# Performance work log

Hardware: AMD Instinct MI355X
Metric: run time of the kernel (lower is better)

Reference implementation:

```python
import jax, jax.numpy as jnp
import numpy as np
from jax import lax

B, N = 8, 8192
H, W = 512, 512
C = 192          # backbone feature channels (Swin-L stage 1)
HF, WF = 128, 128  # H/4, W/4
STATE = 256
VLR = 3
STRIDE = 4.0
DOWN = 4.0
EPS = 1e-8


def bilinear_sample(feat, poly, h, w):
    """F.grid_sample(align_corners=True, bilinear) equivalent.
    feat: (B,C,h,w), poly: (B,N,2) pixel coords -> (B,C,N)."""
    gx = poly[..., 0] / (w / 2.0) - 1.0
    gy = poly[..., 1] / (h / 2.0) - 1.0
    x = (gx + 1.0) * 0.5 * (w - 1)   # align_corners=True unnormalize
    y = (gy + 1.0) * 0.5 * (h - 1)
    x0 = jnp.floor(x); y0 = jnp.floor(y)
    fx = x - x0; fy = y - y0
    x0i = jnp.clip(x0, 0, w - 1).astype(jnp.int32)
    x1i = jnp.clip(x0 + 1, 0, w - 1).astype(jnp.int32)
    y0i = jnp.clip(y0, 0, h - 1).astype(jnp.int32)
    y1i = jnp.clip(y0 + 1, 0, h - 1).astype(jnp.int32)
    b = jnp.arange(feat.shape[0])[:, None]
    f00 = feat[b, :, y0i, x0i]  # (B,N,C)
    f01 = feat[b, :, y0i, x1i]
    f10 = feat[b, :, y1i, x0i]
    f11 = feat[b, :, y1i, x1i]
    w00 = ((1 - fy) * (1 - fx))[..., None]
    w01 = ((1 - fy) * fx)[..., None]
    w10 = (fy * (1 - fx))[..., None]
    w11 = (fy * fx)[..., None]
    out = f00 * w00 + f01 * w01 + f10 * w10 + f11 * w11  # (B,N,C)
    return jnp.transpose(out, (0, 2, 1))  # (B,C,N)


def mlp3(x, W1, b1, W2, b2, W3, b3):
    """per-point MLP (1x1 conv stack). x: (B,Cin,N) -> (B,Cout,N)."""
    h1 = jax.nn.relu(jnp.einsum('oc,bcn->bon', W1, x) + b1[None, :, None])
    h2 = jax.nn.relu(jnp.einsum('oc,bcn->bon', W2, h1) + b2[None, :, None])
    return jnp.einsum('oc,bcn->bon', W3, h2) + b3[None, :, None]


def can_poly(poly, mask):
    # canonical poly: subtract per-polygon masked min of valid points
    big = jnp.float32(1e9)
    masked = jnp.where(mask[..., None] > 0, poly, big)
    mins = jnp.min(masked, axis=1, keepdims=True)  # (B,1,2)
    return (poly - mins) * mask[..., None]


def polygon_angles(poly, mask):
    prev = jnp.roll(poly, 1, axis=1)
    nxt = jnp.roll(poly, -1, axis=1)
    v1 = prev - poly
    v2 = nxt - poly
    dot = jnp.sum(v1 * v2, axis=-1)
    nrm = jnp.linalg.norm(v1, axis=-1) * jnp.linalg.norm(v2, axis=-1)
    cosang = jnp.clip(dot / (nrm + EPS), -1.0, 1.0)
    return jnp.arccos(cosang) * mask  # (B,N)


def setup_inputs() -> dict:
    key = jax.random.key(0)
    ks = jax.random.split(key, 20)
    DIN_OFF = C + 2   # 194
    DIN_CLS = C + 3   # 195
    inp = {
        'image': jax.random.normal(ks[0], (B, 3, H, W), jnp.float32),
        'pred_points': jax.random.uniform(ks[1], (B, N, 2), jnp.float32) * (WF - 1),
        'valid_mask': jnp.ones((B, N), jnp.float32),
        'bw': jax.random.normal(ks[2], (C, 3, 4, 4), jnp.float32) * 0.05,
        'bb': jnp.zeros((C,), jnp.float32),
        'off_W1': jax.random.normal(ks[3], (VLR, STATE, DIN_OFF), jnp.float32) * 0.02,
        'off_b1': jnp.zeros((VLR, STATE), jnp.float32),
        'off_W2': jax.random.normal(ks[4], (VLR, STATE, STATE), jnp.float32) * 0.02,
        'off_b2': jnp.zeros((VLR, STATE), jnp.float32),
        'off_W3': jax.random.normal(ks[5], (VLR, 2, STATE), jnp.float32) * 0.02,
        'off_b3': jnp.zeros((VLR, 2), jnp.float32),
        'cls_W1': jax.random.normal(ks[6], (STATE, DIN_CLS), jnp.float32) * 0.02,
        'cls_b1': jnp.zeros((STATE,), jnp.float32),
        'cls_W2': jax.random.normal(ks[7], (STATE, STATE), jnp.float32) * 0.02,
        'cls_b2': jnp.zeros((STATE,), jnp.float32),
        'cls_W3': jax.random.normal(ks[8], (1, STATE), jnp.float32) * 0.02,
        'cls_b3': jnp.zeros((1,), jnp.float32),
    }
    return inp


def reference(image, pred_points, valid_mask, bw, bb,
              off_W1, off_b1, off_W2, off_b2, off_W3, off_b3,
              cls_W1, cls_b1, cls_W2, cls_b2, cls_W3, cls_b3):
    # frozen backbone stand-in (torch.no_grad on swin_l): stride-4 patch-embed conv
    feat = lax.conv_general_dilated(
        image, bw, window_strides=(4, 4), padding='VALID',
        dimension_numbers=('NCHW', 'OIHW', 'NCHW')) + bb[None, :, None, None]
    feat = lax.stop_gradient(feat)  # (B,C,HF,WF)

    py = pred_points
    for i in range(VLR):
        c_py = can_poly(py, valid_mask)
        g = bilinear_sample(feat, py, HF, WF) * valid_mask[:, None, :]   # (B,C,N)
        x = jnp.concatenate([g, jnp.transpose(c_py, (0, 2, 1))], axis=1)  # (B,C+2,N)
        off = mlp3(x, off_W1[i], off_b1[i], off_W2[i], off_b2[i], off_W3[i], off_b3[i])
        off = jnp.transpose(off, (0, 2, 1)) * valid_mask[..., None]      # (B,N,2)
        py = py + off * STRIDE

    gf = bilinear_sample(feat, py, HF, WF) * valid_mask[:, None, :]      # (B,C,N)
    angles = lax.stop_gradient(polygon_angles(py, valid_mask))           # (B,N)
    cls_feat = jnp.concatenate(
        [gf, jnp.transpose(py, (0, 2, 1)), angles[:, None, :]], axis=1)  # (B,C+3,N)
    logits = mlp3(cls_feat, cls_W1, cls_b1, cls_W2, cls_b2, cls_W3, cls_b3)  # (B,1,N)
    cls_points = logits[:, 0, :] * valid_mask                            # (B,N)

    final_refined_points = py * DOWN
    return (final_refined_points, cls_points)
```

## Files before the change

### kernel.cpp

```cpp
#include <hip/hip_runtime.h>
#include <hip/hip_bf16.h>
#include <hip/hip_fp8.h>

#define NB 8
#define NP 8192
#define IMH 512
#define IMW 512
#define NC 192
#define FH 128
#define FW 128
#define NSTATE 256

#define P1 232
#define P2 264
#define K1PAD 224
#define CPITCH 72
#define W1FRAG 57344
#define W2FRAG 65536

typedef __attribute__((ext_vector_type(8))) unsigned short ush8;
typedef __attribute__((ext_vector_type(8))) short short8v;
typedef __attribute__((ext_vector_type(4))) float f32x4;

__device__ __forceinline__ float bf2f(unsigned short u) {
  return __uint_as_float(((unsigned)u) << 16);
}
__device__ __forceinline__ float fp8tof(unsigned char b) {
  __hip_fp8_e4m3 v;
  v.__x = b;
  return (float)v;
}
__device__ __forceinline__ unsigned char ftofp8(float f) {
  __hip_fp8_e4m3 v(f);
  return v.__x;
}
__device__ __forceinline__ unsigned fenc(float f) {
  unsigned u = __float_as_uint(f);
  return (u & 0x80000000u) ? ~u : (u | 0x80000000u);
}
__device__ __forceinline__ float fdec(unsigned u) {
  return __uint_as_float((u & 0x80000000u) ? (u & 0x7FFFFFFFu) : ~u);
}

__global__ __launch_bounds__(256) void conv_kernel(
    const float* __restrict__ img, const __hip_bfloat16* __restrict__ wcb,
    const float* __restrict__ bb, unsigned char* __restrict__ feat) {
  __shared__ __hip_bfloat16 Xim[64 * CPITCH];

  const int tid = threadIdx.x;
  const int lane = tid & 63;
  const int w = tid >> 6;
  const int cl = lane & 15;
  const int kg = lane >> 4;
  const int b = blockIdx.x & 7;
  const int pix0 = (blockIdx.x >> 3) * 64;
  const int y = pix0 >> 7;
  const int xh = (pix0 >> 6) & 1;

  {
    const int pix = tid & 63;
    const int q = tid >> 6;
    *(uint2*)&Xim[pix * CPITCH + 48 + q * 4] = (uint2){0u, 0u};
  }

#pragma unroll
  for (int it = 0; it < 3; ++it) {
    const int idx = it * 256 + tid;
    const int row = idx >> 6;
    const int c = idx & 63;
    const int ci = row >> 2, ky = row & 3;
    const float4 v = *(const float4*)(img + (((size_t)b * 3 + ci) * IMH +
                                             (y * 4 + ky)) * IMW + xh * 256 + c * 4);
    __hip_bfloat16 h[4];
    h[0] = __float2bfloat16(v.x);
    h[1] = __float2bfloat16(v.y);
    h[2] = __float2bfloat16(v.z);
    h[3] = __float2bfloat16(v.w);
    *(uint2*)&Xim[c * CPITCH + ci * 16 + ky * 4] = *(const uint2*)h;
  }
  __syncthreads();

  f32x4 acc[4][3];
#pragma unroll
  for (int mt = 0; mt < 4; ++mt)
#pragma unroll
    for (int nt = 0; nt < 3; ++nt) acc[mt][nt] = (f32x4){0, 0, 0, 0};

#pragma unroll
  for (int kc = 0; kc < 2; ++kc) {
    short8v af[4], bfv[3];
#pragma unroll
    for (int mt = 0; mt < 4; ++mt)
      af[mt] = *(const short8v*)&Xim[(mt * 16 + cl) * CPITCH + kc * 32 + kg * 8];
#pragma unroll
    for (int nt = 0; nt < 3; ++nt)
      bfv[nt] = *(const short8v*)&wcb[(size_t)(w * 48 + nt * 16 + cl) * 64 +
                                      kc * 32 + kg * 8];
#pragma unroll
    for (int mt = 0; mt < 4; ++mt)
#pragma unroll
      for (int nt = 0; nt < 3; ++nt)
        acc[mt][nt] = __builtin_amdgcn_mfma_f32_16x16x32_bf16(
            af[mt], bfv[nt], acc[mt][nt], 0, 0, 0);
  }

#pragma unroll
  for (int nt = 0; nt < 3; ++nt) {
    const float bias = bb[w * 48 + nt * 16 + cl];
#pragma unroll
    for (int mt = 0; mt < 4; ++mt) {
#pragma unroll
      for (int r = 0; r < 4; ++r) {
        feat[((size_t)(w * 8 + b) * 16384 + pix0 + mt * 16 + kg * 4 + r) * 48 +
             nt * 16 + cl] = ftofp8(acc[mt][nt][r] + bias);
      }
    }
  }
}

__global__ void prep_all_kernel(
    const float* __restrict__ oW1, const float* __restrict__ cW1,
    const float* __restrict__ oW2, const float* __restrict__ cW2,
    const float* __restrict__ bw, const float* __restrict__ pred,
    const float* __restrict__ mask, __hip_bfloat16* __restrict__ w1c,
    __hip_bfloat16* __restrict__ w2c, __hip_bfloat16* __restrict__ wcb,
    unsigned* __restrict__ mins4) {
  __shared__ float sx[4], sy[4];
  const int idx = blockIdx.x * 256 + threadIdx.x;
  const int region = blockIdx.y;
  if (region == 0) {
    if (idx >= 4 * W1FRAG) return;
    const int L = idx / W1FRAG;
    const int rem = idx - L * W1FRAG;
    const int kc = rem >> 13;
    const int r2 = rem & 8191;
    const int ng = r2 >> 9;
    const int r3 = r2 & 511;
    const int lane = r3 >> 3;
    const int e = r3 & 7;
    const int n = ng * 16 + (lane & 15);
    const int k = kc * 32 + (lane >> 4) * 8 + e;
    const float* src = (L < 3) ? (oW1 + (size_t)L * 256 * 194) : cW1;
    const int K = (L < 3) ? 194 : 195;
    w1c[idx] = __float2bfloat16((k < K) ? src[(size_t)n * K + k] : 0.0f);
  } else if (region == 1) {
    if (idx >= 4 * W2FRAG) return;
    const int L = idx >> 16;
    const int rem = idx & 65535;
    const int kc = rem >> 13;
    const int r2 = rem & 8191;
    const int ng = r2 >> 9;
    const int r3 = r2 & 511;
    const int lane = r3 >> 3;
    const int e = r3 & 7;
    const int n = ng * 16 + (lane & 15);
    const int k = kc * 32 + (lane >> 4) * 8 + e;
    const float* src = (L < 3) ? (oW2 + (size_t)L * 65536) : cW2;
    w2c[idx] = __float2bfloat16(src[(size_t)n * 256 + k]);
  } else if (region == 2) {
    if (idx < 48) mins4[16 + idx] = fenc(1e9f);
    if (idx >= 192 * 64) return;
    const int n = idx >> 6;
    const int k = idx & 63;
    wcb[idx] = __float2bfloat16((k < 48) ? bw[(size_t)n * 48 + k] : 0.0f);
  } else {
    if (blockIdx.x >= 8) return;
    const int b = blockIdx.x;
    float mx = 1e9f, my = 1e9f;
    for (int n = threadIdx.x; n < NP; n += 256) {
      float m = mask[(size_t)b * NP + n];
      float2 p = *(const float2*)&pred[((size_t)b * NP + n) * 2];
      mx = fminf(mx, m > 0.0f ? p.x : 1e9f);
      my = fminf(my, m > 0.0f ? p.y : 1e9f);
    }
#pragma unroll
    for (int o = 32; o > 0; o >>= 1) {
      mx = fminf(mx, __shfl_down(mx, o));
      my = fminf(my, __shfl_down(my, o));
    }
    if ((threadIdx.x & 63) == 0) {
      sx[threadIdx.x >> 6] = mx;
      sy[threadIdx.x >> 6] = my;
    }
    __syncthreads();
    if (threadIdx.x == 0) {
      mx = fminf(fminf(sx[0], sx[1]), fminf(sx[2], sx[3]));
      my = fminf(fminf(sy[0], sy[1]), fminf(sy[2], sy[3]));
      mins4[b * 2 + 0] = fenc(mx);
      mins4[b * 2 + 1] = fenc(my);
    }
  }
}

template <bool CLS>
__global__ __launch_bounds__(256, 4) void mlp_kernel(
    const unsigned char* __restrict__ feat,
    const float* __restrict__ p_in,
    const float* __restrict__ mask,
    const unsigned* __restrict__ mins_in,
    unsigned* __restrict__ mins_out,
    const __hip_bfloat16* __restrict__ W1c, const float* __restrict__ b1,
    const __hip_bfloat16* __restrict__ W2c, const float* __restrict__ b2,
    const float* __restrict__ W3, const float* __restrict__ b3,
    float* __restrict__ out0) {
  __shared__ __hip_bfloat16 Xls[64 * P2];
  __shared__ float red[4][64][2];

  const int tid = threadIdx.x;
  const int lane = tid & 63;
  const int w = tid >> 6;
  const int cl = lane & 15;
  const int kg = lane >> 4;
  const int b = blockIdx.x & 7;
  const int m0 = (blockIdx.x >> 3) * 64;

  {
    const int m = tid >> 2;
    const int j = tid & 3;
    const int n = m0 + m;
    const size_t pidx = (size_t)b * NP + n;
    const float msk = mask[pidx];
    const float2 pv = *(const float2*)&p_in[pidx * 2];
    const float px = pv.x, pyv = pv.y;
    const float xs = px * (127.0f / 128.0f);
    const float ys = pyv * (127.0f / 128.0f);
    const float x0f = floorf(xs), y0f = floorf(ys);
    const float fx = xs - x0f, fy = ys - y0f;
    const int x0 = (int)fminf(fmaxf(x0f, 0.0f), 127.0f);
    const int x1 = (int)fminf(fmaxf(x0f + 1.0f, 0.0f), 127.0f);
    const int y0 = (int)fminf(fmaxf(y0f, 0.0f), 127.0f);
    const int y1 = (int)fminf(fmaxf(y0f + 1.0f, 0.0f), 127.0f);
    const float w00 = (1.0f - fy) * (1.0f - fx);
    const float w01 = (1.0f - fy) * fx;
    const float w10 = fy * (1.0f - fx);
    const float w11 = fy * fx;
    const unsigned char* fb = feat + (size_t)(j * 8 + b) * 16384 * 48;
    const uint4* r00 = (const uint4*)(fb + (size_t)(y0 * FW + x0) * 48);
    const uint4* r01 = (const uint4*)(fb + (size_t)(y0 * FW + x1) * 48);
    const uint4* r10 = (const uint4*)(fb + (size_t)(y1 * FW + x0) * 48);
    const uint4* r11 = (const uint4*)(fb + (size_t)(y1 * FW + x1) * 48);
#pragma unroll
    for (int v = 0; v < 3; ++v) {
      union { uint4 u; unsigned char c[16]; } a0, a1, a2, a3;
      a0.u = r00[v]; a1.u = r01[v]; a2.u = r10[v]; a3.u = r11[v];
      __hip_bfloat16 h[16];
#pragma unroll
      for (int e = 0; e < 16; ++e) {
        float gg = w00 * fp8tof(a0.c[e]) + w01 * fp8tof(a1.c[e]) +
                   w10 * fp8tof(a2.c[e]) + w11 * fp8tof(a3.c[e]);
        h[e] = __float2bfloat16(gg * msk);
      }
      *(ush8*)&Xls[m * P1 + j * 48 + v * 16 + 0] = *(const ush8*)&h[0];
      *(ush8*)&Xls[m * P1 + j * 48 + v * 16 + 8] = *(const ush8*)&h[8];
    }
    if (j == 0) {
      __hip_bfloat16 ex[32];
#pragma unroll
      for (int i = 0; i < 32; ++i) ex[i] = __float2bfloat16(0.0f);
      if constexpr (!CLS) {
        ex[0] = __float2bfloat16((px - fdec(mins_in[b * 2 + 0])) * msk);
        ex[1] = __float2bfloat16((pyv - fdec(mins_in[b * 2 + 1])) * msk);
      } else {
        ex[0] = __float2bfloat16(px);
        ex[1] = __float2bfloat16(pyv);
        const int npv = (n + NP - 1) & (NP - 1);
        const int nnx = (n + 1) & (NP - 1);
        const float2 pp = *(const float2*)&p_in[((size_t)b * NP + npv) * 2];
        const float2 pn = *(const float2*)&p_in[((size_t)b * NP + nnx) * 2];
        const float v1x = pp.x - px, v1y = pp.y - pyv;
        const float v2x = pn.x - px, v2y = pn.y - pyv;
        const float dot = v1x * v2x + v1y * v2y;
        const float nrm =
            sqrtf(v1x * v1x + v1y * v1y) * sqrtf(v2x * v2x + v2y * v2y);
        const float ca = fminf(fmaxf(dot / (nrm + 1e-8f), -1.0f), 1.0f);
        ex[2] = __float2bfloat16(acosf(ca) * msk);
      }
#pragma unroll
      for (int q = 0; q < 4; ++q)
        *(ush8*)&Xls[m * P1 + 192 + q * 8] = *(const ush8*)&ex[q * 8];
    }
  }

  float b1v[4], b2v[4], w3av[4], w3bv[4];
#pragma unroll
  for (int nt = 0; nt < 4; ++nt) {
    const int n = w * 64 + nt * 16 + cl;
    b1v[nt] = b1[n];
    b2v[nt] = b2[n];
    w3av[nt] = W3[n];
    w3bv[nt] = CLS ? 0.0f : W3[256 + n];
  }
  __syncthreads();

  f32x4 acc[4][4];
#pragma unroll
  for (int mt = 0; mt < 4; ++mt)
#pragma unroll
    for (int nt = 0; nt < 4; ++nt) acc[mt][nt] = (f32x4){0, 0, 0, 0};

#pragma unroll
  for (int kc = 0; kc < 7; ++kc) {
    short8v af[4], bfv[4];
#pragma unroll
    for (int nt = 0; nt < 4; ++nt)
      bfv[nt] = *(const short8v*)&W1c[kc * 8192 + (w * 4 + nt) * 512 + lane * 8];
#pragma unroll
    for (int mt = 0; mt < 4; ++mt)
      af[mt] = *(const short8v*)&Xls[(mt * 16 + cl) * P1 + kc * 32 + kg * 8];
#pragma unroll
    for (int mt = 0; mt < 4; ++mt)
#pragma unroll
      for (int nt = 0; nt < 4; ++nt)
        acc[mt][nt] = __builtin_amdgcn_mfma_f32_16x16x32_bf16(
            af[mt], bfv[nt], acc[mt][nt], 0, 0, 0);
  }
  __syncthreads();

#pragma unroll
  for (int nt = 0; nt < 4; ++nt) {
    const float bias = b1v[nt];
    const int n = w * 64 + nt * 16 + cl;
#pragma unroll
    for (int mt = 0; mt < 4; ++mt) {
#pragma unroll
      for (int r = 0; r < 4; ++r) {
        const float v = fmaxf(acc[mt][nt][r] + bias, 0.0f);
        Xls[(mt * 16 + kg * 4 + r) * P2 + n] = __float2bfloat16(v);
      }
    }
  }
  __syncthreads();

  f32x4 acc2[4][4];
#pragma unroll
  for (int mt = 0; mt < 4; ++mt)
#pragma unroll
    for (int nt = 0; nt < 4; ++nt) acc2[mt][nt] = (f32x4){0, 0, 0, 0};

#pragma unroll
  for (int kc = 0; kc < 8; ++kc) {
    short8v af[4], bfv[4];
#pragma unroll
    for (int nt = 0; nt < 4; ++nt)
      bfv[nt] = *(const short8v*)&W2c[kc * 8192 + (w * 4 + nt) * 512 + lane * 8];
#pragma unroll
    for (int mt = 0; mt < 4; ++mt)
      af[mt] = *(const short8v*)&Xls[(mt * 16 + cl) * P2 + kc * 32 + kg * 8];
#pragma unroll
    for (int mt = 0; mt < 4; ++mt)
#pragma unroll
      for (int nt = 0; nt < 4; ++nt)
        acc2[mt][nt] = __builtin_amdgcn_mfma_f32_16x16x32_bf16(
            af[mt], bfv[nt], acc2[mt][nt], 0, 0, 0);
  }

  float pr[4][4][2];
#pragma unroll
  for (int mt = 0; mt < 4; ++mt)
#pragma unroll
    for (int r = 0; r < 4; ++r) { pr[mt][r][0] = 0.0f; pr[mt][r][1] = 0.0f; }

#pragma unroll
  for (int nt = 0; nt < 4; ++nt) {
    const float bias = b2v[nt];
    const float w3a = w3av[nt];
    const float w3b = w3bv[nt];
#pragma unroll
    for (int mt = 0; mt < 4; ++mt) {
#pragma unroll
      for (int r = 0; r < 4; ++r) {
        const float t = fmaxf(acc2[mt][nt][r] + bias, 0.0f);
        pr[mt][r][0] = fmaf(t, w3a, pr[mt][r][0]);
        if constexpr (!CLS) pr[mt][r][1] = fmaf(t, w3b, pr[mt][r][1]);
      }
    }
  }
#pragma unroll
  for (int s = 1; s < 16; s <<= 1) {
#pragma unroll
    for (int mt = 0; mt < 4; ++mt)
#pragma unroll
      for (int r = 0; r < 4; ++r) {
        pr[mt][r][0] += __shfl_xor(pr[mt][r][0], s);
        if constexpr (!CLS) pr[mt][r][1] += __shfl_xor(pr[mt][r][1], s);
      }
  }
  if constexpr (!CLS) {
    if (cl < 8) {
      const int r = cl >> 1, o = cl & 1;
#pragma unroll
      for (int mt = 0; mt < 4; ++mt)
        red[w][mt * 16 + kg * 4 + r][o] = pr[mt][r][o];
    }
  } else {
    if (cl < 4) {
      const int r = cl;
#pragma unroll
      for (int mt = 0; mt < 4; ++mt)
        red[w][mt * 16 + kg * 4 + r][0] = pr[mt][r][0];
    }
  }
  __syncthreads();

  if constexpr (!CLS) {
    if (tid < 128) {
      const int m = tid >> 1, o = tid & 1;
      const float s = red[0][m][o] + red[1][m][o] + red[2][m][o] + red[3][m][o];
      const size_t pidx = (size_t)b * NP + m0 + m;
      const float msk = mask[pidx];
      const float off = (s + b3[o]) * msk;
      const float nv = p_in[pidx * 2 + o] + off * 4.0f;
      out0[pidx * 2 + o] = nv;
      float mval = (msk > 0.0f) ? nv : 1e9f;
#pragma unroll
      for (int st = 2; st < 64; st <<= 1)
        mval = fminf(mval, __shfl_xor(mval, st));
      if ((tid & 63) < 2 && mins_out != nullptr)
        atomicMin(&mins_out[b * 2 + o], fenc(mval));
    }
  } else {
    if (tid < 64) {
      const int m = tid;
      const float s = red[0][m][0] + red[1][m][0] + red[2][m][0] + red[3][m][0];
      const size_t pidx = (size_t)b * NP + m0 + m;
      const float msk = mask[pidx];
      out0[pidx * 2 + 0] = p_in[pidx * 2 + 0] * 4.0f;
      out0[pidx * 2 + 1] = p_in[pidx * 2 + 1] * 4.0f;
      out0[(size_t)2 * NB * NP + pidx] = (s + b3[0]) * msk;
    }
  }
}

extern "C" void kernel_launch(void* const* d_in, const int* in_sizes, int n_in,
                              void* d_out, int out_size, void* d_ws,
                              size_t ws_size, hipStream_t stream) {
  const float* image = (const float*)d_in[0];
  const float* pred  = (const float*)d_in[1];
  const float* mask  = (const float*)d_in[2];
  const float* bw    = (const float*)d_in[3];
  const float* bb    = (const float*)d_in[4];
  const float* oW1   = (const float*)d_in[5];
  const float* ob1   = (const float*)d_in[6];
  const float* oW2   = (const float*)d_in[7];
  const float* ob2   = (const float*)d_in[8];
  const float* oW3   = (const float*)d_in[9];
  const float* ob3   = (const float*)d_in[10];
  const float* cW1   = (const float*)d_in[11];
  const float* cb1   = (const float*)d_in[12];
  const float* cW2   = (const float*)d_in[13];
  const float* cb2   = (const float*)d_in[14];
  const float* cW3   = (const float*)d_in[15];
  const float* cb3   = (const float*)d_in[16];
  float* out = (float*)d_out;

  char* ws = (char*)d_ws;
  unsigned char* feat = (unsigned char*)ws;
  const size_t featB = (size_t)NB * FH * FW * NC;
  float* pyA  = (float*)(ws + featB);
  float* pyB  = pyA + (size_t)NB * NP * 2;
  unsigned* mins4 = (unsigned*)(pyB + (size_t)NB * NP * 2);
  __hip_bfloat16* w1c = (__hip_bfloat16*)(mins4 + 64);
  __hip_bfloat16* w2c = w1c + (size_t)4 * W1FRAG;
  __hip_bfloat16* wcb = w2c + (size_t)4 * W2FRAG;

  prep_all_kernel<<<dim3(1024, 4), 256, 0, stream>>>(
      oW1, cW1, oW2, cW2, bw, pred, mask, w1c, w2c, wcb, mins4);
  conv_kernel<<<dim3(NB * 16384 / 64), 256, 0, stream>>>(image, wcb, bb, feat);

  const float* cur = pred;
  float* nxt = pyA;
  for (int i = 0; i < 3; ++i) {
    mlp_kernel<false><<<dim3(NB * NP / 64), 256, 0, stream>>>(
        feat, cur, mask, mins4 + i * 16,
        (i < 2) ? (mins4 + (i + 1) * 16) : nullptr,
        w1c + (size_t)i * W1FRAG, ob1 + (size_t)i * NSTATE,
        w2c + (size_t)i * W2FRAG, ob2 + (size_t)i * NSTATE,
        oW3 + (size_t)i * 2 * NSTATE, ob3 + (size_t)i * 2, nxt);
    cur = nxt;
    nxt = (nxt == pyA) ? pyB : pyA;
  }
  mlp_kernel<true><<<dim3(NB * NP / 64), 256, 0, stream>>>(
      feat, cur, mask, nullptr, nullptr, w1c + (size_t)3 * W1FRAG, cb1,
      w2c + (size_t)3 * W2FRAG, cb2, cW3, cb3, out);
}
```

Measured before the change: 221.5 us.

## Store fp8 features pixel-contiguous across all channels and lower MLP occupancy hint

The conv kernel now writes the fp8 feature map as one 192-byte record per pixel instead of four separate 48-channel planes. The gather in the MLP kernel has its four threads per point read interleaved 16-byte chunks of that record, so each corner fetch touches one contiguous row rather than four distant planes. The launch-bounds minimum-blocks hint drops from 4 to 2, which lets the compiler use more registers per thread at the cost of fewer resident waves. Dead helpers and an unused define are removed.

Result: faster. 186.7 us, median of 3 (-15.7%).

```diff
diff --git a/kernel.cpp b/kernel.cpp
--- a/kernel.cpp
+++ b/kernel.cpp
@@ -13,7 +13,6 @@
 
 #define P1 232
 #define P2 264
-#define K1PAD 224
 #define CPITCH 72
 #define W1FRAG 57344
 #define W2FRAG 65536
@@ -22,9 +21,6 @@
 typedef __attribute__((ext_vector_type(8))) short short8v;
 typedef __attribute__((ext_vector_type(4))) float f32x4;
 
-__device__ __forceinline__ float bf2f(unsigned short u) {
-  return __uint_as_float(((unsigned)u) << 16);
-}
 __device__ __forceinline__ float fp8tof(unsigned char b) {
   __hip_fp8_e4m3 v;
   v.__x = b;
@@ -111,8 +107,8 @@
     for (int mt = 0; mt < 4; ++mt) {
 #pragma unroll
       for (int r = 0; r < 4; ++r) {
-        feat[((size_t)(w * 8 + b) * 16384 + pix0 + mt * 16 + kg * 4 + r) * 48 +
-             nt * 16 + cl] = ftofp8(acc[mt][nt][r] + bias);
+        feat[((size_t)b * 16384 + pix0 + mt * 16 + kg * 4 + r) * 192 +
+             w * 48 + nt * 16 + cl] = ftofp8(acc[mt][nt][r] + bias);
       }
     }
   }
@@ -193,7 +189,7 @@
 }
 
 template <bool CLS>
-__global__ __launch_bounds__(256, 4) void mlp_kernel(
+__global__ __launch_bounds__(256, 2) void mlp_kernel(
     const unsigned char* __restrict__ feat,
     const float* __restrict__ p_in,
     const float* __restrict__ mask,
@@ -216,7 +212,7 @@
 
   {
     const int m = tid >> 2;
-    const int j = tid & 3;
+    const int s = tid & 3;
     const int n = m0 + m;
     const size_t pidx = (size_t)b * NP + n;
     const float msk = mask[pidx];
@@ -234,15 +230,18 @@
     const float w01 = (1.0f - fy) * fx;
     const float w10 = fy * (1.0f - fx);
     const float w11 = fy * fx;
-    const unsigned char* fb = feat + (size_t)(j * 8 + b) * 16384 * 48;
-    const uint4* r00 = (const uint4*)(fb + (size_t)(y0 * FW + x0) * 48);
-    const uint4* r01 = (const uint4*)(fb + (size_t)(y0 * FW + x1) * 48);
-    const uint4* r10 = (const uint4*)(fb + (size_t)(y1 * FW + x0) * 48);
-    const uint4* r11 = (const uint4*)(fb + (size_t)(y1 * FW + x1) * 48);
+    const unsigned char* fb = feat + (size_t)b * 16384 * 192 + s * 16;
+    const unsigned char* r00 = fb + (size_t)(y0 * FW + x0) * 192;
+    const unsigned char* r01 = fb + (size_t)(y0 * FW + x1) * 192;
+    const unsigned char* r10 = fb + (size_t)(y1 * FW + x0) * 192;
+    const unsigned char* r11 = fb + (size_t)(y1 * FW + x1) * 192;
 #pragma unroll
     for (int v = 0; v < 3; ++v) {
       union { uint4 u; unsigned char c[16]; } a0, a1, a2, a3;
-      a0.u = r00[v]; a1.u = r01[v]; a2.u = r10[v]; a3.u = r11[v];
+      a0.u = *(const uint4*)(r00 + v * 64);
+      a1.u = *(const uint4*)(r01 + v * 64);
+      a2.u = *(const uint4*)(r10 + v * 64);
+      a3.u = *(const uint4*)(r11 + v * 64);
       __hip_bfloat16 h[16];
 #pragma unroll
       for (int e = 0; e < 16; ++e) {
@@ -250,10 +249,10 @@
                    w10 * fp8tof(a2.c[e]) + w11 * fp8tof(a3.c[e]);
         h[e] = __float2bfloat16(gg * msk);
       }
-      *(ush8*)&Xls[m * P1 + j * 48 + v * 16 + 0] = *(const ush8*)&h[0];
-      *(ush8*)&Xls[m * P1 + j * 48 + v * 16 + 8] = *(const ush8*)&h[8];
-    }
-    if (j == 0) {
+      *(ush8*)&Xls[m * P1 + v * 64 + s * 16 + 0] = *(const ush8*)&h[0];
+      *(ush8*)&Xls[m * P1 + v * 64 + s * 16 + 8] = *(const ush8*)&h[8];
+    }
+    if (s == 0) {
       __hip_bfloat16 ex[32];
 #pragma unroll
       for (int i = 0; i < 32; ++i) ex[i] = __float2bfloat16(0.0f);
```
